# Optimization experiments

Measured on AMD Instinct MI355X. Metric: run time of the kernel, lower is better.

The kernel has to match this reference:

```python
import jax, jax.numpy as jnp
import numpy as np


def setup_inputs() -> dict:
    key = jax.random.key(0)
    k1, k2 = jax.random.split(key)
    inputs = jax.random.normal(k1, (32768, 512), dtype=jnp.float32)
    codebook = jax.random.normal(k2, (8192, 512), dtype=jnp.float32)
    return {"inputs": inputs, "codebook": codebook}


def reference(inputs, codebook):
    # inputs: [N, D] (flattened), codebook: [K, D]
    D = codebook.shape[1]
    x = inputs.reshape(-1, D)                          # [N, D]
    cb_sqr = jnp.sum(codebook ** 2, axis=1)            # [K]
    x_sqr = jnp.sum(x ** 2, axis=1, keepdims=True)     # [N, 1]
    distances = (cb_sqr[None, :] + x_sqr) - 2.0 * jnp.einsum('nd,kd->nk', x, codebook)
    soft_distances = jax.nn.softmax(-distances, axis=1)  # [N, K]
    return soft_distances
```

## Files before the change

kernel.cpp:

```cpp
#include <hip/hip_runtime.h>


typedef __attribute__((ext_vector_type(8))) __bf16 bf16x8;
typedef __attribute__((ext_vector_type(4))) float f32x4;

typedef __attribute__((address_space(1))) const void global_cvoid;
typedef __attribute__((address_space(3))) void lds_void;

__device__ inline unsigned short f32_to_bf16_rne(float f) {
    unsigned int u = __float_as_uint(f);
    unsigned int r = u + 0x7FFFu + ((u >> 16) & 1u);
    return (unsigned short)(r >> 16);
}
__device__ inline float bf16u_to_f32(unsigned short h) {
    return __uint_as_float(((unsigned int)h) << 16);
}

__global__ void split_kernel(const float* __restrict__ in,
                             unsigned short* __restrict__ hi,
                             unsigned short* __restrict__ lo, int n4) {
    int i = blockIdx.x * blockDim.x + threadIdx.x;
    int stride = gridDim.x * blockDim.x;
    for (; i < n4; i += stride) {
        float4 v = reinterpret_cast<const float4*>(in)[i];
        float vv[4] = {v.x, v.y, v.z, v.w};
        ushort4 hv, lv;
        unsigned short h[4], l[4];
#pragma unroll
        for (int j = 0; j < 4; ++j) {
            h[j] = f32_to_bf16_rne(vv[j]);
            float r = vv[j] - bf16u_to_f32(h[j]);
            l[j] = f32_to_bf16_rne(r);
        }
        hv.x = h[0]; hv.y = h[1]; hv.z = h[2]; hv.w = h[3];
        lv.x = l[0]; lv.y = l[1]; lv.z = l[2]; lv.w = l[3];
        reinterpret_cast<ushort4*>(hi)[i] = hv;
        reinterpret_cast<ushort4*>(lo)[i] = lv;
    }
}

__global__ void rowsq_kernel(const float* __restrict__ cb, float* __restrict__ out) {
    int row = blockIdx.x * 4 + (threadIdx.x >> 6);
    int lane = threadIdx.x & 63;
    const float4* p = reinterpret_cast<const float4*>(cb + (size_t)row * 512);
    float4 a = p[lane];
    float4 b = p[lane + 64];
    float s = a.x * a.x + a.y * a.y + a.z * a.z + a.w * a.w +
              b.x * b.x + b.y * b.y + b.z * b.z + b.w * b.w;
#pragma unroll
    for (int o = 32; o >= 1; o >>= 1) s += __shfl_xor(s, o);
    if (lane == 0) out[row] = s;
}

__global__ __launch_bounds__(256) void gemm_kernel(
    const unsigned short* __restrict__ Ah, const unsigned short* __restrict__ Al,
    const unsigned short* __restrict__ Bh, const unsigned short* __restrict__ Bl,
    const float* __restrict__ cbq, float* __restrict__ out,
    float* __restrict__ max_part, float* __restrict__ sum_part) {
    __shared__ unsigned short smem[4 * 4096];
    __shared__ float sred_max[2][128];
    __shared__ float sred_sum[2][128];

    const int t = threadIdx.x;
    const int lane = t & 63;
    const int w = t >> 6;
    const int wm = w >> 1, wn = w & 1;
    const int fr = lane & 15, fg = lane >> 4;
    const int bid = blockIdx.x;
    const int tm = bid >> 6, tn = bid & 63;
    const int row0 = tm * 128, col0 = tn * 128;

    f32x4 acc[4][4] = {};

    const int s_lrow = t >> 2;
    const int s_kb = (t & 3) * 8;
    const unsigned short* const srcs[4] = {
        Ah + (size_t)row0 * 512, Al + (size_t)row0 * 512,
        Bh + (size_t)col0 * 512, Bl + (size_t)col0 * 512};

    for (int kt = 0; kt < 512; kt += 32) {
#pragma unroll
        for (int tile = 0; tile < 4; ++tile) {
            const unsigned short* base = srcs[tile] + kt + s_kb;
#pragma unroll
            for (int r = 0; r < 2; ++r) {
                const unsigned short* g = base + (size_t)(s_lrow + r * 64) * 512;
                unsigned short* l = smem + tile * 4096 + r * 2048 + w * 512;
                __builtin_amdgcn_global_load_lds((global_cvoid*)g, (lds_void*)l, 16, 0, 0);
            }
        }
        __syncthreads();

        bf16x8 ah[4], al[4], bh[4], bl[4];
#pragma unroll
        for (int m = 0; m < 4; ++m) {
            int ro = (wm * 64 + m * 16 + fr) * 32 + fg * 8;
            ah[m] = *reinterpret_cast<const bf16x8*>(smem + ro);
            al[m] = *reinterpret_cast<const bf16x8*>(smem + 4096 + ro);
        }
#pragma unroll
        for (int n = 0; n < 4; ++n) {
            int co = (wn * 64 + n * 16 + fr) * 32 + fg * 8;
            bh[n] = *reinterpret_cast<const bf16x8*>(smem + 2 * 4096 + co);
            bl[n] = *reinterpret_cast<const bf16x8*>(smem + 3 * 4096 + co);
        }
#pragma unroll
        for (int m = 0; m < 4; ++m)
#pragma unroll
            for (int n = 0; n < 4; ++n) {
                acc[m][n] = __builtin_amdgcn_mfma_f32_16x16x32_bf16(ah[m], bh[n], acc[m][n], 0, 0, 0);
                acc[m][n] = __builtin_amdgcn_mfma_f32_16x16x32_bf16(ah[m], bl[n], acc[m][n], 0, 0, 0);
                acc[m][n] = __builtin_amdgcn_mfma_f32_16x16x32_bf16(al[m], bh[n], acc[m][n], 0, 0, 0);
            }
        __syncthreads();
    }

    float cq[4];
#pragma unroll
    for (int n = 0; n < 4; ++n) cq[n] = cbq[col0 + wn * 64 + n * 16 + fr];

#pragma unroll
    for (int m = 0; m < 4; ++m)
#pragma unroll
        for (int n = 0; n < 4; ++n)
#pragma unroll
            for (int r = 0; r < 4; ++r)
                acc[m][n][r] = 2.0f * acc[m][n][r] - cq[n];

    float rmx[4][4];
#pragma unroll
    for (int m = 0; m < 4; ++m)
#pragma unroll
        for (int r = 0; r < 4; ++r) {
            float v = acc[m][0][r];
#pragma unroll
            for (int n = 1; n < 4; ++n) v = fmaxf(v, acc[m][n][r]);
#pragma unroll
            for (int o = 1; o < 16; o <<= 1) v = fmaxf(v, __shfl_xor(v, o));
            rmx[m][r] = v;
        }
    if (fr == 0) {
#pragma unroll
        for (int m = 0; m < 4; ++m)
#pragma unroll
            for (int r = 0; r < 4; ++r)
                sred_max[wn][wm * 64 + m * 16 + fg * 4 + r] = rmx[m][r];
    }
    __syncthreads();
#pragma unroll
    for (int m = 0; m < 4; ++m)
#pragma unroll
        for (int r = 0; r < 4; ++r) {
            int rl = wm * 64 + m * 16 + fg * 4 + r;
            rmx[m][r] = fmaxf(sred_max[0][rl], sred_max[1][rl]);
        }
    float rsm[4][4];
#pragma unroll
    for (int m = 0; m < 4; ++m)
#pragma unroll
        for (int r = 0; r < 4; ++r) {
            float s = 0.0f;
#pragma unroll
            for (int n = 0; n < 4; ++n) s += __expf(acc[m][n][r] - rmx[m][r]);
#pragma unroll
            for (int o = 1; o < 16; o <<= 1) s += __shfl_xor(s, o);
            rsm[m][r] = s;
        }
    if (fr == 0) {
#pragma unroll
        for (int m = 0; m < 4; ++m)
#pragma unroll
            for (int r = 0; r < 4; ++r)
                sred_sum[wn][wm * 64 + m * 16 + fg * 4 + r] = rsm[m][r];
    }
    __syncthreads();
    if (wn == 0 && fr == 0) {
#pragma unroll
        for (int m = 0; m < 4; ++m)
#pragma unroll
            for (int r = 0; r < 4; ++r) {
                int rl = wm * 64 + m * 16 + fg * 4 + r;
                size_t grow = (size_t)(row0 + rl);
                max_part[grow * 64 + tn] = rmx[m][r];
                sum_part[grow * 64 + tn] = sred_sum[0][rl] + sred_sum[1][rl];
            }
    }
#pragma unroll
    for (int m = 0; m < 4; ++m)
#pragma unroll
        for (int n = 0; n < 4; ++n)
#pragma unroll
            for (int r = 0; r < 4; ++r) {
                size_t grow = (size_t)(row0 + wm * 64 + m * 16 + fg * 4 + r);
                int gcol = col0 + wn * 64 + n * 16 + fr;
                out[grow * 8192 + gcol] = acc[m][n][r];
            }
}

__global__ void combine_kernel(const float* __restrict__ max_part,
                               const float* __restrict__ sum_part,
                               float* __restrict__ row_m, float* __restrict__ row_is) {
    int row = blockIdx.x * 4 + (threadIdx.x >> 6);
    int lane = threadIdx.x & 63;
    size_t off = (size_t)row * 64 + lane;
    float m = max_part[off];
    float s = sum_part[off];
    float gm = m;
#pragma unroll
    for (int o = 32; o >= 1; o >>= 1) gm = fmaxf(gm, __shfl_xor(gm, o));
    float c = s * __expf(m - gm);
#pragma unroll
    for (int o = 32; o >= 1; o >>= 1) c += __shfl_xor(c, o);
    if (lane == 0) {
        row_m[row] = gm;
        row_is[row] = 1.0f / c;
    }
}

__global__ void norm_kernel(float* __restrict__ out, const float* __restrict__ row_m,
                            const float* __restrict__ row_is) {
    size_t i = (size_t)blockIdx.x * blockDim.x + threadIdx.x;
    size_t stride = (size_t)gridDim.x * blockDim.x;
    const size_t n4 = 268435456ull / 4;
    float4* p = reinterpret_cast<float4*>(out);
    for (; i < n4; i += stride) {
        int row = (int)(i >> 11);
        float m = row_m[row];
        float is = row_is[row];
        float4 v = p[i];
        v.x = __expf(v.x - m) * is;
        v.y = __expf(v.y - m) * is;
        v.z = __expf(v.z - m) * is;
        v.w = __expf(v.w - m) * is;
        p[i] = v;
    }
}

extern "C" void kernel_launch(void* const* d_in, const int* in_sizes, int n_in,
                              void* d_out, int out_size, void* d_ws, size_t ws_size,
                              hipStream_t stream) {
    const float* x = (const float*)d_in[0];
    const float* cb = (const float*)d_in[1];
    float* out = (float*)d_out;
    char* ws = (char*)d_ws;

    unsigned short* Xh = (unsigned short*)(ws);
    unsigned short* Xl = (unsigned short*)(ws + 33554432ull);
    unsigned short* Ch = (unsigned short*)(ws + 67108864ull);
    unsigned short* Cl = (unsigned short*)(ws + 75497472ull);
    float* cbq       = (float*)(ws + 83886080ull);
    float* max_part  = (float*)(ws + 83918848ull);
    float* sum_part  = (float*)(ws + 92307456ull);
    float* row_m     = (float*)(ws + 100696064ull);
    float* row_is    = (float*)(ws + 100827136ull);

    split_kernel<<<2048, 256, 0, stream>>>(x, Xh, Xl, 32768 * 512 / 4);
    split_kernel<<<1024, 256, 0, stream>>>(cb, Ch, Cl, 8192 * 512 / 4);
    rowsq_kernel<<<2048, 256, 0, stream>>>(cb, cbq);
    gemm_kernel<<<16384, 256, 0, stream>>>(Xh, Xl, Ch, Cl, cbq, out, max_part, sum_part);
    combine_kernel<<<8192, 256, 0, stream>>>(max_part, sum_part, row_m, row_is);
    norm_kernel<<<4096, 256, 0, stream>>>(out, row_m, row_is);
}
```

Baseline: 1.548 ms.

## Rewrite split-bf16 GEMM with 256x256 tiles, double-buffered swizzled LDS pipeline

The GEMM tile grows from 128x128 to 256x256 with 512 threads (8 waves, 2x4), so each loaded operand is reused across more outputs. The three split-precision products are restructured as 24 stages over the K dimension, each a (hi/lo A, hi/lo B) chunk pair, with prefetch into a double-buffered, XOR-swizzled LDS layout. Fine-grained barriers, vmcnt waits and setprio are added to overlap global-to-LDS loads with MFMA work, and blocks are remapped for L2 locality. The partial softmax statistics shrink to 32 column tiles, and the combine kernel and workspace offsets change to match. The larger tile raises register pressure (8x4 accumulators) and the manual wait and barrier scheme is fragile.

```diff
diff --git a/kernel.cpp b/kernel.cpp
--- a/kernel.cpp
+++ b/kernel.cpp
@@ -14,6 +14,10 @@
 }
 __device__ inline float bf16u_to_f32(unsigned short h) {
     return __uint_as_float(((unsigned int)h) << 16);
+}
+
+__device__ inline int swz_slot(int r, int fg) {
+    return (r >> 1) * 8 + (((fg << 1) | (r & 1)) ^ ((r >> 1) & 7));
 }
 
 __global__ void split_kernel(const float* __restrict__ in,
@@ -52,166 +56,231 @@
     if (lane == 0) out[row] = s;
 }
 
-__global__ __launch_bounds__(256) void gemm_kernel(
+
+#define STAGE_UNIT(tt_, kk_, b_)                                                                  \
+    do {                                                                                          \
+        int prod_ = (tt_) >> 3, ch_ = (tt_) & 7;                                                  \
+        const unsigned short* As_ =                                                               \
+            (prod_ < 2 ? Ah : Al) + (size_t)row0 * 512 + ch_ * 64 + (kk_) * 32;                   \
+        const unsigned short* Bs_ =                                                               \
+            (prod_ == 1 ? Bl : Bh) + (size_t)col0 * 512 + ch_ * 64 + (kk_) * 32;                  \
+        _Pragma("unroll") for (int j = 0; j < 2; ++j)                                             \
+            __builtin_amdgcn_global_load_lds((global_cvoid*)(As_ + (size_t)sr[j] * 512 + sc[j]),  \
+                                             (lds_void*)&lds[b_][0][kk_][sslot[j] * 8], 16, 0, 0); \
+        _Pragma("unroll") for (int j = 0; j < 2; ++j)                                             \
+            __builtin_amdgcn_global_load_lds((global_cvoid*)(Bs_ + (size_t)sr[j] * 512 + sc[j]),  \
+                                             (lds_void*)&lds[b_][1][kk_][sslot[j] * 8], 16, 0, 0); \
+    } while (0)
+
+#define READ_A(kk_, mb_, b_)                                                           \
+    do {                                                                               \
+        _Pragma("unroll") for (int m = 0; m < 4; ++m) {                                \
+            int r_ = wm * 128 + ((mb_) + m) * 16 + fr;                                 \
+            afr[m] = *(const bf16x8*)&lds[b_][0][kk_][swz_slot(r_, fg) * 8];           \
+        }                                                                              \
+    } while (0)
+
+#define READ_B(kk_, b_)                                                                \
+    do {                                                                               \
+        _Pragma("unroll") for (int n = 0; n < 4; ++n) {                                \
+            int r_ = wn * 64 + n * 16 + fr;                                            \
+            bfr[n] = *(const bf16x8*)&lds[b_][1][kk_][swz_slot(r_, fg) * 8];           \
+        }                                                                              \
+    } while (0)
+
+#define MFMA16(mb_)                                                                    \
+    do {                                                                               \
+        _Pragma("unroll") for (int m = 0; m < 4; ++m)                                  \
+            _Pragma("unroll") for (int n = 0; n < 4; ++n)                              \
+                acc[(mb_) + m][n] = __builtin_amdgcn_mfma_f32_16x16x32_bf16(           \
+                    afr[m], bfr[n], acc[(mb_) + m][n], 0, 0, 0);                       \
+    } while (0)
+
+#define MID_SYNC()                                              \
+    do {                                                        \
+        __builtin_amdgcn_s_barrier();                           \
+        asm volatile("s_waitcnt lgkmcnt(0)" ::: "memory");      \
+        __builtin_amdgcn_sched_barrier(0);                      \
+    } while (0)
+
+#define CLOSE_PLAIN()                                           \
+    do {                                                        \
+        __builtin_amdgcn_sched_barrier(0);                      \
+        __builtin_amdgcn_s_barrier();                           \
+        __builtin_amdgcn_sched_barrier(0);                      \
+    } while (0)
+
+#define CLOSE_VM()                                              \
+    do {                                                        \
+        asm volatile("s_waitcnt vmcnt(4)" ::: "memory");        \
+        __builtin_amdgcn_sched_barrier(0);                      \
+        __builtin_amdgcn_s_barrier();                           \
+        __builtin_amdgcn_sched_barrier(0);                      \
+    } while (0)
+
+__global__ __launch_bounds__(512, 2) void gemm_kernel(
     const unsigned short* __restrict__ Ah, const unsigned short* __restrict__ Al,
     const unsigned short* __restrict__ Bh, const unsigned short* __restrict__ Bl,
     const float* __restrict__ cbq, float* __restrict__ out,
     float* __restrict__ max_part, float* __restrict__ sum_part) {
-    __shared__ unsigned short smem[4 * 4096];
-    __shared__ float sred_max[2][128];
-    __shared__ float sred_sum[2][128];
+    __shared__ __align__(16) unsigned short lds[2][2][2][8192];
 
     const int t = threadIdx.x;
     const int lane = t & 63;
     const int w = t >> 6;
-    const int wm = w >> 1, wn = w & 1;
+    const int wm = w >> 2, wn = w & 3;
     const int fr = lane & 15, fg = lane >> 4;
-    const int bid = blockIdx.x;
-    const int tm = bid >> 6, tn = bid & 63;
-    const int row0 = tm * 128, col0 = tn * 128;
-
-    f32x4 acc[4][4] = {};
-
-    const int s_lrow = t >> 2;
-    const int s_kb = (t & 3) * 8;
-    const unsigned short* const srcs[4] = {
-        Ah + (size_t)row0 * 512, Al + (size_t)row0 * 512,
-        Bh + (size_t)col0 * 512, Bl + (size_t)col0 * 512};
-
-    for (int kt = 0; kt < 512; kt += 32) {
-#pragma unroll
-        for (int tile = 0; tile < 4; ++tile) {
-            const unsigned short* base = srcs[tile] + kt + s_kb;
-#pragma unroll
-            for (int r = 0; r < 2; ++r) {
-                const unsigned short* g = base + (size_t)(s_lrow + r * 64) * 512;
-                unsigned short* l = smem + tile * 4096 + r * 2048 + w * 512;
-                __builtin_amdgcn_global_load_lds((global_cvoid*)g, (lds_void*)l, 16, 0, 0);
-            }
-        }
-        __syncthreads();
-
-        bf16x8 ah[4], al[4], bh[4], bl[4];
-#pragma unroll
-        for (int m = 0; m < 4; ++m) {
-            int ro = (wm * 64 + m * 16 + fr) * 32 + fg * 8;
-            ah[m] = *reinterpret_cast<const bf16x8*>(smem + ro);
-            al[m] = *reinterpret_cast<const bf16x8*>(smem + 4096 + ro);
-        }
-#pragma unroll
-        for (int n = 0; n < 4; ++n) {
-            int co = (wn * 64 + n * 16 + fr) * 32 + fg * 8;
-            bh[n] = *reinterpret_cast<const bf16x8*>(smem + 2 * 4096 + co);
-            bl[n] = *reinterpret_cast<const bf16x8*>(smem + 3 * 4096 + co);
-        }
-#pragma unroll
-        for (int m = 0; m < 4; ++m)
-#pragma unroll
-            for (int n = 0; n < 4; ++n) {
-                acc[m][n] = __builtin_amdgcn_mfma_f32_16x16x32_bf16(ah[m], bh[n], acc[m][n], 0, 0, 0);
-                acc[m][n] = __builtin_amdgcn_mfma_f32_16x16x32_bf16(ah[m], bl[n], acc[m][n], 0, 0, 0);
-                acc[m][n] = __builtin_amdgcn_mfma_f32_16x16x32_bf16(al[m], bh[n], acc[m][n], 0, 0, 0);
-            }
-        __syncthreads();
-    }
+
+    int bid = blockIdx.x;
+    int swz = (bid & 7) * 512 + (bid >> 3);
+    const int bm = swz >> 5, bn = swz & 31;
+    const int row0 = bm * 256, col0 = bn * 256;
+
+    int sslot[2], sr[2], sc[2];
+#pragma unroll
+    for (int j = 0; j < 2; ++j) {
+        int slot = j * 512 + t;
+        int pair = slot >> 3, idx = slot & 7;
+        int v = idx ^ (pair & 7);
+        sr[j] = pair * 2 + (v & 1);
+        sc[j] = (v >> 1) * 8;
+        sslot[j] = slot;
+    }
+
+    f32x4 acc[8][4] = {};
+    bf16x8 afr[4], bfr[4];
+
+    STAGE_UNIT(0, 0, 0);
+    STAGE_UNIT(0, 1, 0);
+    asm volatile("s_waitcnt vmcnt(4)" ::: "memory");
+    __builtin_amdgcn_sched_barrier(0);
+    __builtin_amdgcn_s_barrier();
+    __builtin_amdgcn_sched_barrier(0);
+
+    for (int tt = 0; tt < 24; ++tt) {
+        const int cb = tt & 1, nb = cb ^ 1;
+        const bool pf = (tt < 23);
+        READ_A(0, 0, cb);
+        READ_B(0, cb);
+        if (pf) STAGE_UNIT(tt + 1, 0, nb);
+        MID_SYNC();
+        __builtin_amdgcn_s_setprio(1);
+        MFMA16(0);
+        __builtin_amdgcn_s_setprio(0);
+        CLOSE_PLAIN();
+        READ_A(0, 4, cb);
+        MID_SYNC();
+        __builtin_amdgcn_s_setprio(1);
+        MFMA16(4);
+        __builtin_amdgcn_s_setprio(0);
+        CLOSE_VM();
+        READ_A(1, 0, cb);
+        READ_B(1, cb);
+        if (pf) STAGE_UNIT(tt + 1, 1, nb);
+        MID_SYNC();
+        __builtin_amdgcn_s_setprio(1);
+        MFMA16(0);
+        __builtin_amdgcn_s_setprio(0);
+        CLOSE_PLAIN();
+        READ_A(1, 4, cb);
+        MID_SYNC();
+        __builtin_amdgcn_s_setprio(1);
+        MFMA16(4);
+        __builtin_amdgcn_s_setprio(0);
+        CLOSE_VM();
+    }
+
+    float* redm = (float*)&lds[0][0][0][0];
+    float* reds = redm + 1024;
 
     float cq[4];
 #pragma unroll
     for (int n = 0; n < 4; ++n) cq[n] = cbq[col0 + wn * 64 + n * 16 + fr];
-
-#pragma unroll
-    for (int m = 0; m < 4; ++m)
+#pragma unroll
+    for (int m = 0; m < 8; ++m)
 #pragma unroll
         for (int n = 0; n < 4; ++n)
 #pragma unroll
             for (int r = 0; r < 4; ++r)
                 acc[m][n][r] = 2.0f * acc[m][n][r] - cq[n];
 
-    float rmx[4][4];
-#pragma unroll
-    for (int m = 0; m < 4; ++m)
+    float rmx[8][4];
+#pragma unroll
+    for (int m = 0; m < 8; ++m)
 #pragma unroll
         for (int r = 0; r < 4; ++r) {
-            float v = acc[m][0][r];
-#pragma unroll
-            for (int n = 1; n < 4; ++n) v = fmaxf(v, acc[m][n][r]);
+            float v = fmaxf(fmaxf(acc[m][0][r], acc[m][1][r]),
+                            fmaxf(acc[m][2][r], acc[m][3][r]));
 #pragma unroll
             for (int o = 1; o < 16; o <<= 1) v = fmaxf(v, __shfl_xor(v, o));
             rmx[m][r] = v;
         }
     if (fr == 0) {
 #pragma unroll
-        for (int m = 0; m < 4; ++m)
+        for (int m = 0; m < 8; ++m)
 #pragma unroll
             for (int r = 0; r < 4; ++r)
-                sred_max[wn][wm * 64 + m * 16 + fg * 4 + r] = rmx[m][r];
+                redm[wn * 256 + wm * 128 + m * 16 + fg * 4 + r] = rmx[m][r];
     }
     __syncthreads();
 #pragma unroll
-    for (int m = 0; m < 4; ++m)
+    for (int m = 0; m < 8; ++m)
 #pragma unroll
         for (int r = 0; r < 4; ++r) {
-            int rl = wm * 64 + m * 16 + fg * 4 + r;
-            rmx[m][r] = fmaxf(sred_max[0][rl], sred_max[1][rl]);
+            int row = wm * 128 + m * 16 + fg * 4 + r;
+            rmx[m][r] = fmaxf(fmaxf(redm[row], redm[256 + row]),
+                              fmaxf(redm[512 + row], redm[768 + row]));
         }
-    float rsm[4][4];
-#pragma unroll
-    for (int m = 0; m < 4; ++m)
+#pragma unroll
+    for (int m = 0; m < 8; ++m)
 #pragma unroll
         for (int r = 0; r < 4; ++r) {
-            float s = 0.0f;
+            float s = 0.f;
 #pragma unroll
             for (int n = 0; n < 4; ++n) s += __expf(acc[m][n][r] - rmx[m][r]);
 #pragma unroll
             for (int o = 1; o < 16; o <<= 1) s += __shfl_xor(s, o);
-            rsm[m][r] = s;
+            if (fr == 0) reds[wn * 256 + wm * 128 + m * 16 + fg * 4 + r] = s;
         }
-    if (fr == 0) {
-#pragma unroll
-        for (int m = 0; m < 4; ++m)
-#pragma unroll
-            for (int r = 0; r < 4; ++r)
-                sred_sum[wn][wm * 64 + m * 16 + fg * 4 + r] = rsm[m][r];
-    }
     __syncthreads();
     if (wn == 0 && fr == 0) {
 #pragma unroll
-        for (int m = 0; m < 4; ++m)
+        for (int m = 0; m < 8; ++m)
 #pragma unroll
             for (int r = 0; r < 4; ++r) {
-                int rl = wm * 64 + m * 16 + fg * 4 + r;
-                size_t grow = (size_t)(row0 + rl);
-                max_part[grow * 64 + tn] = rmx[m][r];
-                sum_part[grow * 64 + tn] = sred_sum[0][rl] + sred_sum[1][rl];
+                int row = wm * 128 + m * 16 + fg * 4 + r;
+                size_t gr = (size_t)(row0 + row);
+                max_part[gr * 32 + bn] = rmx[m][r];
+                sum_part[gr * 32 + bn] =
+                    reds[row] + reds[256 + row] + reds[512 + row] + reds[768 + row];
             }
     }
 #pragma unroll
-    for (int m = 0; m < 4; ++m)
+    for (int m = 0; m < 8; ++m)
 #pragma unroll
         for (int n = 0; n < 4; ++n)
 #pragma unroll
             for (int r = 0; r < 4; ++r) {
-                size_t grow = (size_t)(row0 + wm * 64 + m * 16 + fg * 4 + r);
-                int gcol = col0 + wn * 64 + n * 16 + fr;
-                out[grow * 8192 + gcol] = acc[m][n][r];
+                size_t gr = (size_t)(row0 + wm * 128 + m * 16 + fg * 4 + r);
+                out[gr * 8192 + col0 + wn * 64 + n * 16 + fr] = acc[m][n][r];
             }
 }
 
 __global__ void combine_kernel(const float* __restrict__ max_part,
                                const float* __restrict__ sum_part,
                                float* __restrict__ row_m, float* __restrict__ row_is) {
-    int row = blockIdx.x * 4 + (threadIdx.x >> 6);
-    int lane = threadIdx.x & 63;
-    size_t off = (size_t)row * 64 + lane;
+    int row = blockIdx.x * 8 + (threadIdx.x >> 5);
+    int l = threadIdx.x & 31;
+    size_t off = (size_t)row * 32 + l;
     float m = max_part[off];
     float s = sum_part[off];
     float gm = m;
 #pragma unroll
-    for (int o = 32; o >= 1; o >>= 1) gm = fmaxf(gm, __shfl_xor(gm, o));
+    for (int o = 16; o >= 1; o >>= 1) gm = fmaxf(gm, __shfl_xor(gm, o, 32));
     float c = s * __expf(m - gm);
 #pragma unroll
-    for (int o = 32; o >= 1; o >>= 1) c += __shfl_xor(c, o);
-    if (lane == 0) {
+    for (int o = 16; o >= 1; o >>= 1) c += __shfl_xor(c, o, 32);
+    if (l == 0) {
         row_m[row] = gm;
         row_is[row] = 1.0f / c;
     }
@@ -250,14 +319,14 @@
     unsigned short* Cl = (unsigned short*)(ws + 75497472ull);
     float* cbq       = (float*)(ws + 83886080ull);
     float* max_part  = (float*)(ws + 83918848ull);
-    float* sum_part  = (float*)(ws + 92307456ull);
-    float* row_m     = (float*)(ws + 100696064ull);
-    float* row_is    = (float*)(ws + 100827136ull);
+    float* sum_part  = (float*)(ws + 88113152ull);
+    float* row_m     = (float*)(ws + 92307456ull);
+    float* row_is    = (float*)(ws + 92438528ull);
 
     split_kernel<<<2048, 256, 0, stream>>>(x, Xh, Xl, 32768 * 512 / 4);
     split_kernel<<<1024, 256, 0, stream>>>(cb, Ch, Cl, 8192 * 512 / 4);
     rowsq_kernel<<<2048, 256, 0, stream>>>(cb, cbq);
-    gemm_kernel<<<16384, 256, 0, stream>>>(Xh, Xl, Ch, Cl, cbq, out, max_part, sum_part);
-    combine_kernel<<<8192, 256, 0, stream>>>(max_part, sum_part, row_m, row_is);
+    gemm_kernel<<<4096, 512, 0, stream>>>(Xh, Xl, Ch, Cl, cbq, out, max_part, sum_part);
+    combine_kernel<<<4096, 256, 0, stream>>>(max_part, sum_part, row_m, row_is);
     norm_kernel<<<4096, 256, 0, stream>>>(out, row_m, row_is);
 }
```

New measurement: 1.732 ms. +11.9%, slower.
